# Kernel optimization log

Hardware: AMD Instinct MI355X
Metric: run time of the kernel (lower is better)

## Reference

```python
import jax, jax.numpy as jnp
import numpy as np

B, CIN, H, W = 16, 15, 256, 256
C, L, M = 64, 4, 16
ENV, D1D = 40, 4
HEAD_IN = C + ENV + D1D
BN_EPS = 1e-5


def setup_inputs() -> dict:
    key = jax.random.key(0)
    ks = iter(jax.random.split(key, 40))
    nrm = lambda shape: jax.random.normal(next(ks), shape, dtype=jnp.float32)
    scale = (2.0 / (C + C)) ** 0.5
    uni = lambda shape: scale * (jax.random.uniform(next(ks), shape, dtype=jnp.float32) - 0.5)
    d = {
        'grid': nrm((B, CIN, H, W)),
        'env': nrm((B, ENV)),
        'd1d': nrm((B, D1D)),
        'lift_w': nrm((C, CIN)) * 0.1, 'lift_b': nrm((C,)) * 0.01,
        'w1r': uni((L, C, C, M, M)), 'w1i': uni((L, C, C, M, M)),
        'w2r': uni((L, C, C, M, M)), 'w2i': uni((L, C, C, M, M)),
        'skip_w': nrm((L, C, C)) * 0.1, 'skip_b': nrm((L, C)) * 0.01,
        'bn_g': jnp.ones((L, C)), 'bn_b': jnp.zeros((L, C)),
        'bn_m': nrm((L, C)) * 0.01, 'bn_v': jnp.abs(nrm((L, C))) * 0.1 + 1.0,
        'proj_w': nrm((C, C)) * 0.1, 'proj_b': nrm((C,)) * 0.01,
        'dw1': nrm((128, HEAD_IN)) * 0.05, 'db1': nrm((128,)) * 0.01,
        'dw2': nrm((64, 128)) * 0.05, 'db2': nrm((64,)) * 0.01,
        'dw3': nrm((8, 64)) * 0.05, 'db3': nrm((8,)) * 0.01,
        'iw1': nrm((128, HEAD_IN)) * 0.05, 'ib1': nrm((128,)) * 0.01,
        'iw2': nrm((64, 128)) * 0.05, 'ib2': nrm((64,)) * 0.01,
        'iw3': nrm((4, 64)) * 0.05, 'ib3': nrm((4,)) * 0.01,
    }
    return d


def _spectral(x, w1, w2):
    # x: [B,C,H,W] real; w1,w2: [C,C,M,M] complex
    h, w = x.shape[-2], x.shape[-1]
    xft = jnp.fft.rfft2(x)  # [B,C,H,W//2+1] complex
    top = jnp.einsum('bixy,ioxy->boxy', xft[:, :, :M, :M], w1)
    bot = jnp.einsum('bixy,ioxy->boxy', xft[:, :, -M:, :M], w2)
    out_ft = jnp.zeros(xft.shape, dtype=xft.dtype)
    out_ft = out_ft.at[:, :, :M, :M].set(top).at[:, :, h - M:, :M].set(bot)
    return jnp.fft.irfft2(out_ft, s=(h, w))


def _conv1x1(x, w, b):
    return jnp.einsum('bchw,oc->bohw', x, w) + b[None, :, None, None]


def _gelu(x):
    return jax.nn.gelu(x, approximate=False)


def reference(grid, env, d1d, lift_w, lift_b, w1r, w1i, w2r, w2i, skip_w, skip_b,
              bn_g, bn_b, bn_m, bn_v, proj_w, proj_b,
              dw1, db1, dw2, db2, dw3, db3, iw1, ib1, iw2, ib2, iw3, ib3):
    x = _gelu(_conv1x1(grid, lift_w, lift_b))
    for l in range(L):
        residual = x
        w1 = w1r[l] + 1j * w1i[l]
        w2 = w2r[l] + 1j * w2i[l]
        y = _spectral(x, w1, w2) + _conv1x1(x, skip_w[l], skip_b[l])
        # BatchNorm2d in eval mode (running stats), dropout is identity at eval
        y = (y - bn_m[l][None, :, None, None]) * jax.lax.rsqrt(bn_v[l] + BN_EPS)[None, :, None, None]
        y = y * bn_g[l][None, :, None, None] + bn_b[l][None, :, None, None]
        x = _gelu(y) + residual
    x = _gelu(_conv1x1(x, proj_w, proj_b))
    x = x.mean(axis=(-2, -1))  # [B,C]
    x = jnp.concatenate([x, env, d1d], axis=-1)  # [B, C+44]
    h = _gelu(x @ dw1.T + db1)
    h = _gelu(h @ dw2.T + db2)
    out_dir = h @ dw3.T + db3
    g = _gelu(x @ iw1.T + ib1)
    g = _gelu(g @ iw2.T + ib2)
    out_int = g @ iw3.T + ib3
    return out_dir, out_int
```

## Files before the change

### kernel.cpp

```cpp
#include <hip/hip_runtime.h>
#include <hip/hip_bf16.h>
#include <math.h>

#define B_ 16
#define CIN_ 15
#define C_ 64
#define L_ 4

typedef __attribute__((ext_vector_type(8))) short short8;
typedef __attribute__((ext_vector_type(4))) short short4v;
typedef __attribute__((ext_vector_type(4))) float f32x4;

__device__ __forceinline__ float gelu_f(float x) {
    float z = fabsf(x) * 0.70710678118654752440f;
    float t = __builtin_amdgcn_rcpf(fmaf(0.3275911f, z, 1.0f));
    float p = t * fmaf(t, fmaf(t, fmaf(t, fmaf(t, 1.061405429f, -1.453152027f), 1.421413741f), -0.284496736f), 0.254829592f);
    float e = __expf(-z * z);
    float E = fmaf(-p, e, 1.0f);
    return 0.5f * fmaf(fabsf(x), E, x);
}

__device__ __forceinline__ unsigned short f2bf(float x) {
    __hip_bfloat16 h = __float2bfloat16(x);
    return *(unsigned short*)&h;
}
__device__ __forceinline__ float bf2f(unsigned short u) {
    __hip_bfloat16 h = *(__hip_bfloat16*)&u;
    return __bfloat162float(h);
}
__device__ __forceinline__ f32x4 mfma16(short8 a, short8 b, f32x4 c) {
    return __builtin_amdgcn_mfma_f32_16x16x32_bf16(a, b, c, 0, 0, 0);
}

#define TWO_PI_OVER_256 0.024543692606170259674f

__global__ __launch_bounds__(256) void k_prep(const float* __restrict__ skip_w,
                                              const float* __restrict__ bn_g, const float* __restrict__ bn_v,
                                              const float* __restrict__ proj_w, const float* __restrict__ lift_w,
                                              unsigned short* __restrict__ TfH, unsigned short* __restrict__ TfL,
                                              unsigned short* __restrict__ TiH, unsigned short* __restrict__ TiL,
                                              unsigned short* __restrict__ WH, unsigned short* __restrict__ WL,
                                              unsigned short* __restrict__ PH, unsigned short* __restrict__ PL,
                                              unsigned short* __restrict__ FcH, unsigned short* __restrict__ FcL,
                                              unsigned short* __restrict__ FsH, unsigned short* __restrict__ FsL,
                                              unsigned short* __restrict__ FnH, unsigned short* __restrict__ FnL,
                                              unsigned short* __restrict__ IcH, unsigned short* __restrict__ IcL,
                                              unsigned short* __restrict__ IsH, unsigned short* __restrict__ IsL,
                                              unsigned short* __restrict__ InH, unsigned short* __restrict__ InL,
                                              unsigned short* __restrict__ LwH, unsigned short* __restrict__ LwL) {
    int id = blockIdx.x * 256 + threadIdx.x;
    if (id < 8192) {
        int col = id >> 8, w = id & 255;
        int kk = (col < 16) ? col : (col - 16);
        float s, c;
        sincosf(TWO_PI_OVER_256 * (float)((w * kk) & 255), &s, &c);
        float v = (col < 16) ? c : -s;
        unsigned short hi = f2bf(v);
        TfH[id] = hi; TfL[id] = f2bf(v - bf2f(hi));
    } else if (id < 16384) {
        int idx = id - 8192;
        int w = idx >> 5, k = idx & 31, ky = k >> 1;
        float s, c;
        sincosf(TWO_PI_OVER_256 * (float)((w * ky) & 255), &s, &c);
        float v = (k & 1) ? -s : c;
        unsigned short hi = f2bf(v);
        TiH[idx] = hi; TiL[idx] = f2bf(v - bf2f(hi));
    } else if (id < 32768) {
        int idx = id - 16384;
        int lco = idx >> 6;
        float scl = bn_g[lco] * rsqrtf(bn_v[lco] + 1e-5f);
        float v = scl * skip_w[idx];
        unsigned short hi = f2bf(v);
        WH[idx] = hi; WL[idx] = f2bf(v - bf2f(hi));
    } else if (id < 36864) {
        int idx = id - 32768;
        float v = proj_w[idx];
        unsigned short hi = f2bf(v);
        PH[idx] = hi; PL[idx] = f2bf(v - bf2f(hi));
    } else if (id < 45056) {
        int idx = id - 36864;
        int j = idx >> 8, h = idx & 255;
        int kxu = j + ((j < 16) ? 0 : 224);
        float s, c;
        sincosf(TWO_PI_OVER_256 * (float)((h * kxu) & 255), &s, &c);
        unsigned short ch = f2bf(c);
        FcH[idx] = ch; FcL[idx] = f2bf(c - bf2f(ch));
        unsigned short sh = f2bf(s);
        unsigned short sl = f2bf(s - bf2f(sh));
        FsH[idx] = sh; FsL[idx] = sl;
        FnH[idx] = sh ^ 0x8000; FnL[idx] = sl ^ 0x8000;
    } else if (id < 53248) {
        int idx = id - 45056;
        int h = idx >> 5, j = idx & 31;
        int kxu = j + ((j < 16) ? 0 : 224);
        float s, c;
        sincosf(TWO_PI_OVER_256 * (float)((h * kxu) & 255), &s, &c);
        unsigned short ch = f2bf(c);
        IcH[idx] = ch; IcL[idx] = f2bf(c - bf2f(ch));
        unsigned short sh = f2bf(s);
        unsigned short sl = f2bf(s - bf2f(sh));
        IsH[idx] = sh; IsL[idx] = sl;
        InH[idx] = sh ^ 0x8000; InL[idx] = sl ^ 0x8000;
    } else if (id < 55296) {
        int idx = id - 53248;
        int co = idx >> 5, k = idx & 31;
        float v = (k < CIN_) ? lift_w[co * CIN_ + k] : 0.0f;
        unsigned short hi = f2bf(v);
        LwH[idx] = hi; LwL[idx] = f2bf(v - bf2f(hi));
    }
}

__global__ __launch_bounds__(256) void k_lift(const float* __restrict__ g,
                                              const unsigned short* __restrict__ LwH, const unsigned short* __restrict__ LwL,
                                              const float* __restrict__ lb, unsigned short* __restrict__ X,
                                              const unsigned short* __restrict__ TfH, const unsigned short* __restrict__ TfL,
                                              float2* __restrict__ Y) {
    __shared__ unsigned short xl[64 * 264];
    __shared__ float lbs[C_];
    int b = blockIdx.x >> 8, h = blockIdx.x & 255;
    int t = threadIdx.x;
    if (t < C_) lbs[t] = lb[t];
    int wv = t >> 6, ln = t & 63;
    int lx = ln & 15, q = ln >> 4;
    short8 bwh[4], bwl[4];
    #pragma unroll
    for (int mt = 0; mt < 4; mt++) {
        bwh[mt] = *(const short8*)(LwH + (mt * 16 + lx) * 32 + q * 8);
        bwl[mt] = *(const short8*)(LwL + (mt * 16 + lx) * 32 + q * 8);
    }
    __syncthreads();
    const float* gb = g + ((size_t)(b * CIN_) * 256 + h) * 256;
    #pragma unroll 1
    for (int nt = 0; nt < 4; nt++) {
        int w0 = wv * 64 + nt * 16;
        int w = w0 + lx;
        short8 agh = {0, 0, 0, 0, 0, 0, 0, 0};
        short8 agl = {0, 0, 0, 0, 0, 0, 0, 0};
        #pragma unroll
        for (int j = 0; j < 8; j++) {
            int ci = q * 8 + j;
            if (ci < CIN_) {
                float v = gb[(size_t)ci * 65536 + w];
                unsigned short hv = f2bf(v);
                agh[j] = (short)hv;
                agl[j] = (short)f2bf(v - bf2f(hv));
            }
        }
        f32x4 acc[4];
        #pragma unroll
        for (int mt = 0; mt < 4; mt++) acc[mt] = (f32x4){0.f, 0.f, 0.f, 0.f};
        #pragma unroll
        for (int mt = 0; mt < 4; mt++) {
            acc[mt] = mfma16(agh, bwh[mt], acc[mt]);
            acc[mt] = mfma16(agh, bwl[mt], acc[mt]);
            acc[mt] = mfma16(agl, bwh[mt], acc[mt]);
        }
        #pragma unroll
        for (int mt = 0; mt < 4; mt++) {
            int co = mt * 16 + lx;
            float bias = lbs[co];
            short4v nw;
            #pragma unroll
            for (int r = 0; r < 4; r++)
                nw[r] = (short)f2bf(gelu_f(acc[mt][r] + bias));
            *(short4v*)(&xl[co * 264 + w0 + q * 4]) = nw;
        }
    }
    __syncthreads();
    {
        f32x4 fa0 = {0.f, 0.f, 0.f, 0.f}, fa1 = {0.f, 0.f, 0.f, 0.f};
        for (int ks = 0; ks < 8; ks++) {
            int k0 = ks * 32;
            short8 a = *(const short8*)(&xl[(wv * 16 + lx) * 264 + k0 + q * 8]);
            short8 bh0 = *(const short8*)(TfH + lx * 256 + k0 + q * 8);
            short8 bl0 = *(const short8*)(TfL + lx * 256 + k0 + q * 8);
            short8 bh1 = *(const short8*)(TfH + (16 + lx) * 256 + k0 + q * 8);
            short8 bl1 = *(const short8*)(TfL + (16 + lx) * 256 + k0 + q * 8);
            fa0 = mfma16(a, bh0, fa0); fa0 = mfma16(a, bl0, fa0);
            fa1 = mfma16(a, bh1, fa1); fa1 = mfma16(a, bl1, fa1);
        }
        #pragma unroll
        for (int r = 0; r < 4; r++) {
            int c = wv * 16 + q * 4 + r;
            Y[(b * 64 + c) * 4096 + h * 16 + lx] = make_float2(fa0[r], fa1[r]);
        }
    }
    unsigned short* Xg = X + (size_t)(b * 256 + h) * 16384;
    #pragma unroll
    for (int r = 0; r < 8; r++) {
        int idx = r * 256 + t;
        int c = idx >> 5, w8 = idx & 31;
        *(short8*)(Xg + idx * 8) = *(const short8*)(&xl[c * 264 + w8 * 8]);
    }
}

__global__ __launch_bounds__(256) void k_fwd_h(const float2* __restrict__ Y, float2* __restrict__ XF,
                                               const unsigned short* __restrict__ FcH, const unsigned short* __restrict__ FcL,
                                               const unsigned short* __restrict__ FsH, const unsigned short* __restrict__ FsL,
                                               const unsigned short* __restrict__ FnH, const unsigned short* __restrict__ FnL) {
    __shared__ float red[4][2][2][64][4];
    int bc = blockIdx.x;
    int t = threadIdx.x;
    int wv = t >> 6, l = t & 63, lx = l & 15, g = l >> 4;
    const float2* Yb = Y + (size_t)bc * 4096;
    f32x4 aR[2], aI[2];
    aR[0] = (f32x4){0.f,0.f,0.f,0.f}; aR[1] = aR[0]; aI[0] = aR[0]; aI[1] = aR[0];
    #pragma unroll
    for (int kk = 0; kk < 2; kk++) {
        int ks = wv * 2 + kk;
        short8 yrh, yrl, yih, yil;
        #pragma unroll
        for (int j = 0; j < 8; j++) {
            float2 v = Yb[(ks * 32 + g * 8 + j) * 16 + lx];
            unsigned short h1 = f2bf(v.x);
            yrh[j] = (short)h1; yrl[j] = (short)f2bf(v.x - bf2f(h1));
            unsigned short h2 = f2bf(v.y);
            yih[j] = (short)h2; yil[j] = (short)f2bf(v.y - bf2f(h2));
        }
        #pragma unroll
        for (int rt = 0; rt < 2; rt++) {
            int base = (rt * 16 + lx) * 256 + ks * 32 + g * 8;
            short8 ch = *(const short8*)(FcH + base);
            short8 cl = *(const short8*)(FcL + base);
            short8 sh = *(const short8*)(FsH + base);
            short8 sl = *(const short8*)(FsL + base);
            short8 nh = *(const short8*)(FnH + base);
            short8 nl = *(const short8*)(FnL + base);
            aR[rt] = mfma16(ch, yrh, aR[rt]);
            aR[rt] = mfma16(ch, yrl, aR[rt]);
            aR[rt] = mfma16(cl, yrh, aR[rt]);
            aR[rt] = mfma16(sh, yih, aR[rt]);
            aR[rt] = mfma16(sh, yil, aR[rt]);
            aR[rt] = mfma16(sl, yih, aR[rt]);
            aI[rt] = mfma16(ch, yih, aI[rt]);
            aI[rt] = mfma16(ch, yil, aI[rt]);
            aI[rt] = mfma16(cl, yih, aI[rt]);
            aI[rt] = mfma16(nh, yrh, aI[rt]);
            aI[rt] = mfma16(nh, yrl, aI[rt]);
            aI[rt] = mfma16(nl, yrh, aI[rt]);
        }
    }
    #pragma unroll
    for (int rt = 0; rt < 2; rt++) {
        *(f32x4*)&red[wv][rt][0][l][0] = aR[rt];
        *(f32x4*)&red[wv][rt][1][l][0] = aI[rt];
    }
    __syncthreads();
    if (t < 128) {
        int rt = t >> 6, ll = t & 63;
        int llx = ll & 15, gg = ll >> 4;
        f32x4 R = *(const f32x4*)&red[0][rt][0][ll][0];
        f32x4 I = *(const f32x4*)&red[0][rt][1][ll][0];
        #pragma unroll
        for (int w = 1; w < 4; w++) {
            R += *(const f32x4*)&red[w][rt][0][ll][0];
            I += *(const f32x4*)&red[w][rt][1][ll][0];
        }
        #pragma unroll
        for (int r = 0; r < 4; r++) {
            int j = rt * 16 + gg * 4 + r;
            XF[(j * 16 + llx) * 1024 + bc] = make_float2(R[r], I[r]);
        }
    }
}

__global__ __launch_bounds__(256) void k_repack(const float* __restrict__ w1r, const float* __restrict__ w1i,
                                                const float* __restrict__ w2r, const float* __restrict__ w2i,
                                                float2* __restrict__ WPK, int l) {
    int j = blockIdx.x >> 6, i = blockIdx.x & 63;
    int t = threadIdx.x;
    int ky = t & 15, o0 = (t >> 4) * 4;
    int x = j & 15;
    const float* wr = (j < 16) ? w1r : w2r;
    const float* wi = (j < 16) ? w1i : w2i;
    size_t sb = ((size_t)(l * 64 + i) * 64 + o0) * 256 + x * 16 + ky;
    float r0 = wr[sb];       float v0 = wi[sb];
    float r1 = wr[sb + 256]; float v1 = wi[sb + 256];
    float r2 = wr[sb + 512]; float v2 = wi[sb + 512];
    float r3 = wr[sb + 768]; float v3 = wi[sb + 768];
    float4* dst = (float4*)(WPK + ((size_t)(j * 16 + ky) * 64 + i) * 64 + o0);
    dst[0] = make_float4(r0, v0, r1, v1);
    dst[1] = make_float4(r2, v2, r3, v3);
}

__global__ __launch_bounds__(256) void k_mix(const float2* __restrict__ XF, const float2* __restrict__ WPK,
                                             float2* __restrict__ YF) {
    __shared__ float2 xs[1024];
    __shared__ float2 wls[4096];
    int s = blockIdx.x;
    int t = threadIdx.x;
    for (int idx = t; idx < 1024; idx += 256) xs[idx] = XF[s * 1024 + idx];
    for (int idx = t; idx < 4096; idx += 256) wls[idx] = WPK[(size_t)s * 4096 + idx];
    __syncthreads();
    int o = t & 63, bg = t >> 6;
    float2 acc[4];
    #pragma unroll
    for (int q = 0; q < 4; q++) acc[q] = make_float2(0.f, 0.f);
    for (int i = 0; i < 64; i++) {
        float2 wv = wls[i * 64 + o];
        #pragma unroll
        for (int q = 0; q < 4; q++) {
            float2 xv = xs[(bg * 4 + q) * 64 + i];
            acc[q].x += xv.x * wv.x - xv.y * wv.y;
            acc[q].y += xv.x * wv.y + xv.y * wv.x;
        }
    }
    #pragma unroll
    for (int q = 0; q < 4; q++) {
        int b = bg * 4 + q;
        YF[(b * 64 + o) * 512 + s] = acc[q];
    }
}

__global__ __launch_bounds__(256) void k_inv_h(const float2* __restrict__ YF, float2* __restrict__ Z,
                                               const unsigned short* __restrict__ IcH, const unsigned short* __restrict__ IcL,
                                               const unsigned short* __restrict__ IsH, const unsigned short* __restrict__ IsL,
                                               const unsigned short* __restrict__ InH, const unsigned short* __restrict__ InL) {
    int bc = blockIdx.x;
    int t = threadIdx.x;
    int wv = t >> 6, l = t & 63, lx = l & 15, g = l >> 4;
    const float2* Yb = YF + (size_t)bc * 512;
    short8 xrh, xrl, xih, xil;
    #pragma unroll
    for (int jj = 0; jj < 8; jj++) {
        float2 v = Yb[(g * 8 + jj) * 16 + lx];
        unsigned short h1 = f2bf(v.x);
        xrh[jj] = (short)h1; xrl[jj] = (short)f2bf(v.x - bf2f(h1));
        unsigned short h2 = f2bf(v.y);
        xih[jj] = (short)h2; xil[jj] = (short)f2bf(v.y - bf2f(h2));
    }
    float2* Zb = Z + (size_t)bc * 4096;
    #pragma unroll
    for (int hh = 0; hh < 4; hh++) {
        int ht = wv * 4 + hh;
        int base = (ht * 16 + lx) * 32 + g * 8;
        short8 ch = *(const short8*)(IcH + base);
        short8 cl = *(const short8*)(IcL + base);
        short8 sh = *(const short8*)(IsH + base);
        short8 sl = *(const short8*)(IsL + base);
        short8 nh = *(const short8*)(InH + base);
        short8 nl = *(const short8*)(InL + base);
        f32x4 aR = {0.f,0.f,0.f,0.f}, aI = {0.f,0.f,0.f,0.f};
        aR = mfma16(ch, xrh, aR); aR = mfma16(ch, xrl, aR); aR = mfma16(cl, xrh, aR);
        aR = mfma16(nh, xih, aR); aR = mfma16(nh, xil, aR); aR = mfma16(nl, xih, aR);
        aI = mfma16(sh, xrh, aI); aI = mfma16(sh, xrl, aI); aI = mfma16(sl, xrh, aI);
        aI = mfma16(ch, xih, aI); aI = mfma16(ch, xil, aI); aI = mfma16(cl, xih, aI);
        #pragma unroll
        for (int r = 0; r < 4; r++) {
            int h = ht * 16 + g * 4 + r;
            Zb[h * 16 + lx] = make_float2(aR[r], aI[r]);
        }
    }
}

__global__ __launch_bounds__(256) void k_tail(unsigned short* __restrict__ X, const float2* __restrict__ Z,
                                              const unsigned short* __restrict__ WH, const unsigned short* __restrict__ WL,
                                              const float* __restrict__ sbl, const float* __restrict__ bng,
                                              const float* __restrict__ bnb, const float* __restrict__ bnm,
                                              const float* __restrict__ bnv,
                                              const unsigned short* __restrict__ TiH, const unsigned short* __restrict__ TiL,
                                              const unsigned short* __restrict__ TfH, const unsigned short* __restrict__ TfL,
                                              float2* __restrict__ Y, int mode,
                                              const unsigned short* __restrict__ PH, const unsigned short* __restrict__ PL,
                                              const float* __restrict__ pb, float* __restrict__ ACC) {
    __shared__ unsigned short xl[64 * 264];
    __shared__ float cbs[64];
    __shared__ float pacc[64];
    __shared__ float pbs[64];
    int b = blockIdx.x >> 8, h = blockIdx.x & 255;
    int t = threadIdx.x;
    unsigned short* Xg = X + (size_t)(b * 256 + h) * 16384;
    #pragma unroll
    for (int r = 0; r < 8; r++) {
        int idx = r * 256 + t;
        int c = idx >> 5, w8 = idx & 31;
        *(short8*)(&xl[c * 264 + w8 * 8]) = *(const short8*)(Xg + idx * 8);
    }
    if (t < 64) {
        float scl = bng[t] * rsqrtf(bnv[t] + 1e-5f);
        cbs[t] = scl * (sbl[t] - bnm[t]) + bnb[t];
        pacc[t] = 0.f;
        pbs[t] = pb[t];
    }
    __syncthreads();

    int wv = t >> 6, ln = t & 63;
    int lx = ln & 15, q = ln >> 4;

    short8 azh[4], azl[4];
    {
        const float2* Zg = Z + (size_t)(b * 64) * 4096 + h * 16;
        #pragma unroll
        for (int mt = 0; mt < 4; mt++) {
            int co = mt * 16 + lx;
            float scl = bng[co] * rsqrtf(bnv[co] + 1e-5f);
            float f2v = scl * (2.0f / 65536.0f);
            float f0 = (q == 0) ? (scl * (1.0f / 65536.0f)) : f2v;
            const float4* zp = (const float4*)(Zg + (size_t)co * 4096 + q * 4);
            float4 z0 = zp[0], z1 = zp[1];
            float v[8];
            v[0] = z0.x * f0;  v[1] = z0.y * f0;
            v[2] = z0.z * f2v; v[3] = z0.w * f2v;
            v[4] = z1.x * f2v; v[5] = z1.y * f2v;
            v[6] = z1.z * f2v; v[7] = z1.w * f2v;
            #pragma unroll
            for (int j = 0; j < 8; j++) {
                unsigned short hv = f2bf(v[j]);
                azh[mt][j] = (short)hv;
                azl[mt][j] = (short)f2bf(v[j] - bf2f(hv));
            }
        }
    }

    short8 tah = *(const short8*)(TiH + (wv * 64 + lx) * 32 + q * 8);
    short8 tal = *(const short8*)(TiL + (wv * 64 + lx) * 32 + q * 8);
    #pragma unroll 1
    for (int nt = 0; nt < 4; nt++) {
        int w0 = wv * 64 + nt * 16;
        int w = w0 + lx;
        short8 tah_c = tah, tal_c = tal;
        if (nt < 3) {
            tah = *(const short8*)(TiH + (w + 16) * 32 + q * 8);
            tal = *(const short8*)(TiL + (w + 16) * 32 + q * 8);
        }
        f32x4 acc[4];
        #pragma unroll
        for (int mt = 0; mt < 4; mt++) acc[mt] = (f32x4){0.f, 0.f, 0.f, 0.f};
        #pragma unroll
        for (int mt = 0; mt < 4; mt++) {
            acc[mt] = mfma16(tah_c, azh[mt], acc[mt]);
            acc[mt] = mfma16(tah_c, azl[mt], acc[mt]);
            acc[mt] = mfma16(tal_c, azh[mt], acc[mt]);
        }
        #pragma unroll
        for (int ks = 0; ks < 2; ks++) {
            int k0 = ks * 32;
            short8 afr;
            #pragma unroll
            for (int j = 0; j < 8; j++)
                afr[j] = (short)xl[(k0 + q * 8 + j) * 264 + w];
            #pragma unroll
            for (int mt = 0; mt < 4; mt++) {
                short8 bh = *(const short8*)(WH + (mt * 16 + lx) * 64 + k0 + q * 8);
                short8 bl = *(const short8*)(WL + (mt * 16 + lx) * 64 + k0 + q * 8);
                acc[mt] = mfma16(afr, bh, acc[mt]);
                acc[mt] = mfma16(afr, bl, acc[mt]);
            }
        }
        #pragma unroll
        for (int mt = 0; mt < 4; mt++) {
            int co = mt * 16 + lx;
            float cb = cbs[co];
            unsigned short* xp = &xl[co * 264 + w0 + q * 4];
            short4v old = *(const short4v*)xp;
            short4v nw;
            #pragma unroll
            for (int r = 0; r < 4; r++) {
                float y = acc[mt][r] + cb;
                float v = gelu_f(y) + bf2f((unsigned short)old[r]);
                nw[r] = (short)f2bf(v);
            }
            *(short4v*)xp = nw;
        }
    }
    __syncthreads();

    if (mode == 1) {
        f32x4 fa0 = {0.f, 0.f, 0.f, 0.f}, fa1 = {0.f, 0.f, 0.f, 0.f};
        for (int ks = 0; ks < 8; ks++) {
            int k0 = ks * 32;
            short8 a = *(const short8*)(&xl[(wv * 16 + lx) * 264 + k0 + q * 8]);
            short8 bh0 = *(const short8*)(TfH + lx * 256 + k0 + q * 8);
            short8 bl0 = *(const short8*)(TfL + lx * 256 + k0 + q * 8);
            short8 bh1 = *(const short8*)(TfH + (16 + lx) * 256 + k0 + q * 8);
            short8 bl1 = *(const short8*)(TfL + (16 + lx) * 256 + k0 + q * 8);
            fa0 = mfma16(a, bh0, fa0); fa0 = mfma16(a, bl0, fa0);
            fa1 = mfma16(a, bh1, fa1); fa1 = mfma16(a, bl1, fa1);
        }
        #pragma unroll
        for (int r = 0; r < 4; r++) {
            int c = wv * 16 + q * 4 + r;
            Y[(b * 64 + c) * 4096 + h * 16 + lx] = make_float2(fa0[r], fa1[r]);
        }
        #pragma unroll
        for (int r = 0; r < 8; r++) {
            int idx = r * 256 + t;
            int c = idx >> 5, w8 = idx & 31;
            *(short8*)(Xg + idx * 8) = *(const short8*)(&xl[c * 264 + w8 * 8]);
        }
    } else {
        float psum[4][4];
        #pragma unroll
        for (int mt = 0; mt < 4; mt++)
            #pragma unroll
            for (int r = 0; r < 4; r++) psum[mt][r] = 0.f;
        #pragma unroll 1
        for (int nt = 0; nt < 4; nt++) {
            int w = wv * 64 + nt * 16 + lx;
            f32x4 acc[4];
            #pragma unroll
            for (int mt = 0; mt < 4; mt++) acc[mt] = (f32x4){0.f, 0.f, 0.f, 0.f};
            #pragma unroll
            for (int ks = 0; ks < 2; ks++) {
                int k0 = ks * 32;
                short8 afr;
                #pragma unroll
                for (int j = 0; j < 8; j++)
                    afr[j] = (short)xl[(k0 + q * 8 + j) * 264 + w];
                #pragma unroll
                for (int mt = 0; mt < 4; mt++) {
                    short8 bh = *(const short8*)(PH + (mt * 16 + lx) * 64 + k0 + q * 8);
                    short8 bl = *(const short8*)(PL + (mt * 16 + lx) * 64 + k0 + q * 8);
                    acc[mt] = mfma16(afr, bh, acc[mt]);
                    acc[mt] = mfma16(afr, bl, acc[mt]);
                }
            }
            #pragma unroll
            for (int mt = 0; mt < 4; mt++) {
                int co = mt * 16 + lx;
                #pragma unroll
                for (int r = 0; r < 4; r++)
                    psum[mt][r] += gelu_f(acc[mt][r] + pbs[co]);
            }
        }
        #pragma unroll
        for (int mt = 0; mt < 4; mt++) {
            int co = mt * 16 + lx;
            float s = psum[mt][0] + psum[mt][1] + psum[mt][2] + psum[mt][3];
            s += __shfl_xor(s, 16, 64);
            s += __shfl_xor(s, 32, 64);
            if (q == 0) atomicAdd(&pacc[co], s);
        }
        __syncthreads();
        if (t < 64) atomicAdd(&ACC[b * 64 + t], pacc[t]);
    }
}

__global__ __launch_bounds__(128) void k_head(const float* __restrict__ ACC, const float* __restrict__ env,
                                              const float* __restrict__ d1d,
                                              const float* __restrict__ dw1, const float* __restrict__ db1,
                                              const float* __restrict__ dw2, const float* __restrict__ db2,
                                              const float* __restrict__ dw3, const float* __restrict__ db3,
                                              const float* __restrict__ iw1, const float* __restrict__ ib1,
                                              const float* __restrict__ iw2, const float* __restrict__ ib2,
                                              const float* __restrict__ iw3, const float* __restrict__ ib3,
                                              float* __restrict__ out) {
    __shared__ float xc[108];
    __shared__ float h1[128];
    __shared__ float h2[64];
    int b = blockIdx.x, t = threadIdx.x;
    if (t < 64) xc[t] = ACC[b * 64 + t] * (1.0f / 65536.0f);
    else if (t < 104) xc[t] = env[b * 40 + (t - 64)];
    else if (t < 108) xc[t] = d1d[b * 4 + (t - 104)];
    __syncthreads();
    {
        float a = db1[t];
        for (int k = 0; k < 108; k++) a += xc[k] * dw1[t * 108 + k];
        h1[t] = gelu_f(a);
    }
    __syncthreads();
    if (t < 64) {
        float a = db2[t];
        for (int k = 0; k < 128; k++) a += h1[k] * dw2[t * 128 + k];
        h2[t] = gelu_f(a);
    }
    __syncthreads();
    if (t < 8) {
        float a = db3[t];
        for (int k = 0; k < 64; k++) a += h2[k] * dw3[t * 64 + k];
        out[b * 8 + t] = a;
    }
    __syncthreads();
    {
        float a = ib1[t];
        for (int k = 0; k < 108; k++) a += xc[k] * iw1[t * 108 + k];
        h1[t] = gelu_f(a);
    }
    __syncthreads();
    if (t < 64) {
        float a = ib2[t];
        for (int k = 0; k < 128; k++) a += h1[k] * iw2[t * 128 + k];
        h2[t] = gelu_f(a);
    }
    __syncthreads();
    if (t < 4) {
        float a = ib3[t];
        for (int k = 0; k < 64; k++) a += h2[k] * iw3[t * 64 + k];
        out[128 + b * 4 + t] = a;
    }
}

extern "C" void kernel_launch(void* const* d_in, const int* in_sizes, int n_in,
                              void* d_out, int out_size, void* d_ws, size_t ws_size,
                              hipStream_t stream) {
    const float* grid_  = (const float*)d_in[0];
    const float* env    = (const float*)d_in[1];
    const float* d1d    = (const float*)d_in[2];
    const float* lift_w = (const float*)d_in[3];
    const float* lift_b = (const float*)d_in[4];
    const float* w1r    = (const float*)d_in[5];
    const float* w1i    = (const float*)d_in[6];
    const float* w2r    = (const float*)d_in[7];
    const float* w2i    = (const float*)d_in[8];
    const float* skip_w = (const float*)d_in[9];
    const float* skip_b = (const float*)d_in[10];
    const float* bn_g   = (const float*)d_in[11];
    const float* bn_b   = (const float*)d_in[12];
    const float* bn_m   = (const float*)d_in[13];
    const float* bn_v   = (const float*)d_in[14];
    const float* proj_w = (const float*)d_in[15];
    const float* proj_b = (const float*)d_in[16];
    const float* dw1 = (const float*)d_in[17];
    const float* db1 = (const float*)d_in[18];
    const float* dw2 = (const float*)d_in[19];
    const float* db2 = (const float*)d_in[20];
    const float* dw3 = (const float*)d_in[21];
    const float* db3 = (const float*)d_in[22];
    const float* iw1 = (const float*)d_in[23];
    const float* ib1 = (const float*)d_in[24];
    const float* iw2 = (const float*)d_in[25];
    const float* ib2 = (const float*)d_in[26];
    const float* iw3 = (const float*)d_in[27];
    const float* ib3 = (const float*)d_in[28];

    char* ws = (char*)d_ws;
    unsigned short* X   = (unsigned short*)(ws);
    float2* S   = (float2*)(ws + 134217728);
    float2* XF  = (float2*)(ws + 167772160);
    float2* YF  = (float2*)(ws + 171966464);
    float2* WPK = (float2*)(ws + 176160768);
    float*  ACC = (float*)(ws + 192937984);
    unsigned short* TfH = (unsigned short*)(ws + 192942080);
    unsigned short* TfL = (unsigned short*)(ws + 192958464);
    unsigned short* TiH = (unsigned short*)(ws + 192974848);
    unsigned short* TiL = (unsigned short*)(ws + 192991232);
    unsigned short* WH  = (unsigned short*)(ws + 193007616);
    unsigned short* WL  = (unsigned short*)(ws + 193040384);
    unsigned short* PH  = (unsigned short*)(ws + 193073152);
    unsigned short* PL  = (unsigned short*)(ws + 193081344);
    unsigned short* FcH = (unsigned short*)(ws + 193089536);
    unsigned short* FcL = (unsigned short*)(ws + 193105920);
    unsigned short* FsH = (unsigned short*)(ws + 193122304);
    unsigned short* FsL = (unsigned short*)(ws + 193138688);
    unsigned short* FnH = (unsigned short*)(ws + 193155072);
    unsigned short* FnL = (unsigned short*)(ws + 193171456);
    unsigned short* IcH = (unsigned short*)(ws + 193187840);
    unsigned short* IcL = (unsigned short*)(ws + 193204224);
    unsigned short* IsH = (unsigned short*)(ws + 193220608);
    unsigned short* IsL = (unsigned short*)(ws + 193236992);
    unsigned short* InH = (unsigned short*)(ws + 193253376);
    unsigned short* InL = (unsigned short*)(ws + 193269760);
    unsigned short* LwH = (unsigned short*)(ws + 193286144);
    unsigned short* LwL = (unsigned short*)(ws + 193290240);

    hipMemsetAsync(ACC, 0, 1024 * sizeof(float), stream);
    k_prep<<<216, 256, 0, stream>>>(skip_w, bn_g, bn_v, proj_w, lift_w,
                                    TfH, TfL, TiH, TiL, WH, WL, PH, PL,
                                    FcH, FcL, FsH, FsL, FnH, FnL, IcH, IcL, IsH, IsL, InH, InL,
                                    LwH, LwL);
    k_lift<<<4096, 256, 0, stream>>>(grid_, LwH, LwL, lift_b, X, TfH, TfL, S);
    for (int l = 0; l < L_; l++) {
        k_repack<<<2048, 256, 0, stream>>>(w1r, w1i, w2r, w2i, WPK, l);
        k_fwd_h<<<1024, 256, 0, stream>>>(S, XF, FcH, FcL, FsH, FsL, FnH, FnL);
        k_mix<<<512, 256, 0, stream>>>(XF, WPK, YF);
        k_inv_h<<<1024, 256, 0, stream>>>(YF, S, IcH, IcL, IsH, IsL, InH, InL);
        k_tail<<<4096, 256, 0, stream>>>(X, S, WH + l * 4096, WL + l * 4096,
                                         skip_b + l * 64, bn_g + l * 64, bn_b + l * 64,
                                         bn_m + l * 64, bn_v + l * 64,
                                         TiH, TiL, TfH, TfL, S, (l < 3) ? 1 : 2,
                                         PH, PL, proj_b, ACC);
    }
    k_head<<<16, 128, 0, stream>>>(ACC, env, d1d, dw1, db1, dw2, db2, dw3, db3,
                                   iw1, ib1, iw2, ib2, iw3, ib3, (float*)d_out);
}
```

Measured before the change: 1.121 ms.

## Split lift across channel halves and pre-split BN-scaled bf16 in inverse FFT

```diff
diff --git a/kernel.cpp b/kernel.cpp
--- a/kernel.cpp
+++ b/kernel.cpp
@@ -115,18 +115,19 @@
                                               const float* __restrict__ lb, unsigned short* __restrict__ X,
                                               const unsigned short* __restrict__ TfH, const unsigned short* __restrict__ TfL,
                                               float2* __restrict__ Y) {
-    __shared__ unsigned short xl[64 * 264];
+    __shared__ unsigned short xl[32 * 264];
     __shared__ float lbs[C_];
-    int b = blockIdx.x >> 8, h = blockIdx.x & 255;
+    int b = blockIdx.x >> 9, h = (blockIdx.x >> 1) & 255, ch = blockIdx.x & 1;
     int t = threadIdx.x;
     if (t < C_) lbs[t] = lb[t];
     int wv = t >> 6, ln = t & 63;
     int lx = ln & 15, q = ln >> 4;
-    short8 bwh[4], bwl[4];
-    #pragma unroll
-    for (int mt = 0; mt < 4; mt++) {
-        bwh[mt] = *(const short8*)(LwH + (mt * 16 + lx) * 32 + q * 8);
-        bwl[mt] = *(const short8*)(LwL + (mt * 16 + lx) * 32 + q * 8);
+    int cob = ch * 32;
+    short8 bwh[2], bwl[2];
+    #pragma unroll
+    for (int mt = 0; mt < 2; mt++) {
+        bwh[mt] = *(const short8*)(LwH + (cob + mt * 16 + lx) * 32 + q * 8);
+        bwl[mt] = *(const short8*)(LwL + (cob + mt * 16 + lx) * 32 + q * 8);
     }
     __syncthreads();
     const float* gb = g + ((size_t)(b * CIN_) * 256 + h) * 256;
@@ -146,28 +147,28 @@
                 agl[j] = (short)f2bf(v - bf2f(hv));
             }
         }
-        f32x4 acc[4];
-        #pragma unroll
-        for (int mt = 0; mt < 4; mt++) acc[mt] = (f32x4){0.f, 0.f, 0.f, 0.f};
-        #pragma unroll
-        for (int mt = 0; mt < 4; mt++) {
+        f32x4 acc[2];
+        #pragma unroll
+        for (int mt = 0; mt < 2; mt++) acc[mt] = (f32x4){0.f, 0.f, 0.f, 0.f};
+        #pragma unroll
+        for (int mt = 0; mt < 2; mt++) {
             acc[mt] = mfma16(agh, bwh[mt], acc[mt]);
             acc[mt] = mfma16(agh, bwl[mt], acc[mt]);
             acc[mt] = mfma16(agl, bwh[mt], acc[mt]);
         }
         #pragma unroll
-        for (int mt = 0; mt < 4; mt++) {
-            int co = mt * 16 + lx;
-            float bias = lbs[co];
+        for (int mt = 0; mt < 2; mt++) {
+            int cl = mt * 16 + lx;
+            float bias = lbs[cob + cl];
             short4v nw;
             #pragma unroll
             for (int r = 0; r < 4; r++)
                 nw[r] = (short)f2bf(gelu_f(acc[mt][r] + bias));
-            *(short4v*)(&xl[co * 264 + w0 + q * 4]) = nw;
-        }
-    }
-    __syncthreads();
-    {
+            *(short4v*)(&xl[cl * 264 + w0 + q * 4]) = nw;
+        }
+    }
+    __syncthreads();
+    if (wv < 2) {
         f32x4 fa0 = {0.f, 0.f, 0.f, 0.f}, fa1 = {0.f, 0.f, 0.f, 0.f};
         for (int ks = 0; ks < 8; ks++) {
             int k0 = ks * 32;
@@ -181,13 +182,13 @@
         }
         #pragma unroll
         for (int r = 0; r < 4; r++) {
-            int c = wv * 16 + q * 4 + r;
+            int c = cob + wv * 16 + q * 4 + r;
             Y[(b * 64 + c) * 4096 + h * 16 + lx] = make_float2(fa0[r], fa1[r]);
         }
     }
-    unsigned short* Xg = X + (size_t)(b * 256 + h) * 16384;
-    #pragma unroll
-    for (int r = 0; r < 8; r++) {
+    unsigned short* Xg = X + (size_t)(b * 256 + h) * 16384 + ch * 8192;
+    #pragma unroll
+    for (int r = 0; r < 4; r++) {
         int idx = r * 256 + t;
         int c = idx >> 5, w8 = idx & 31;
         *(short8*)(Xg + idx * 8) = *(const short8*)(&xl[c * 264 + w8 * 8]);
@@ -312,10 +313,11 @@
     }
 }
 
-__global__ __launch_bounds__(256) void k_inv_h(const float2* __restrict__ YF, float2* __restrict__ Z,
+__global__ __launch_bounds__(256) void k_inv_h(const float2* __restrict__ YF, unsigned short* __restrict__ Zs,
                                                const unsigned short* __restrict__ IcH, const unsigned short* __restrict__ IcL,
                                                const unsigned short* __restrict__ IsH, const unsigned short* __restrict__ IsL,
-                                               const unsigned short* __restrict__ InH, const unsigned short* __restrict__ InL) {
+                                               const unsigned short* __restrict__ InH, const unsigned short* __restrict__ InL,
+                                               const float* __restrict__ bng, const float* __restrict__ bnv) {
     int bc = blockIdx.x;
     int t = threadIdx.x;
     int wv = t >> 6, l = t & 63, lx = l & 15, g = l >> 4;
@@ -329,7 +331,9 @@
         unsigned short h2 = f2bf(v.y);
         xih[jj] = (short)h2; xil[jj] = (short)f2bf(v.y - bf2f(h2));
     }
-    float2* Zb = Z + (size_t)bc * 4096;
+    int c = bc & 63;
+    float s = bng[c] * rsqrtf(bnv[c] + 1e-5f) * ((lx == 0) ? (1.0f / 65536.0f) : (2.0f / 65536.0f));
+    unsigned short* Zb = Zs + (size_t)bc * 16384;
     #pragma unroll
     for (int hh = 0; hh < 4; hh++) {
         int ht = wv * 4 + hh;
@@ -348,12 +352,16 @@
         #pragma unroll
         for (int r = 0; r < 4; r++) {
             int h = ht * 16 + g * 4 + r;
-            Zb[h * 16 + lx] = make_float2(aR[r], aI[r]);
-        }
-    }
-}
-
-__global__ __launch_bounds__(256) void k_tail(unsigned short* __restrict__ X, const float2* __restrict__ Z,
+            float vR = aR[r] * s, vI = aI[r] * s;
+            unsigned short hR = f2bf(vR), hI = f2bf(vI);
+            unsigned short lR = f2bf(vR - bf2f(hR)), lI = f2bf(vI - bf2f(hI));
+            ((unsigned int*)(Zb + h * 64))[lx]      = (unsigned)hR | ((unsigned)hI << 16);
+            ((unsigned int*)(Zb + h * 64 + 32))[lx] = (unsigned)lR | ((unsigned)lI << 16);
+        }
+    }
+}
+
+__global__ __launch_bounds__(256) void k_tail(unsigned short* __restrict__ X, const unsigned short* __restrict__ Zs,
                                               const unsigned short* __restrict__ WH, const unsigned short* __restrict__ WL,
                                               const float* __restrict__ sbl, const float* __restrict__ bng,
                                               const float* __restrict__ bnb, const float* __restrict__ bnm,
@@ -389,26 +397,12 @@
 
     short8 azh[4], azl[4];
     {
-        const float2* Zg = Z + (size_t)(b * 64) * 4096 + h * 16;
+        const unsigned short* Zg = Zs + (size_t)(b * 64) * 16384 + h * 64;
         #pragma unroll
         for (int mt = 0; mt < 4; mt++) {
-            int co = mt * 16 + lx;
-            float scl = bng[co] * rsqrtf(bnv[co] + 1e-5f);
-            float f2v = scl * (2.0f / 65536.0f);
-            float f0 = (q == 0) ? (scl * (1.0f / 65536.0f)) : f2v;
-            const float4* zp = (const float4*)(Zg + (size_t)co * 4096 + q * 4);
-            float4 z0 = zp[0], z1 = zp[1];
-            float v[8];
-            v[0] = z0.x * f0;  v[1] = z0.y * f0;
-            v[2] = z0.z * f2v; v[3] = z0.w * f2v;
-            v[4] = z1.x * f2v; v[5] = z1.y * f2v;
-            v[6] = z1.z * f2v; v[7] = z1.w * f2v;
-            #pragma unroll
-            for (int j = 0; j < 8; j++) {
-                unsigned short hv = f2bf(v[j]);
-                azh[mt][j] = (short)hv;
-                azl[mt][j] = (short)f2bf(v[j] - bf2f(hv));
-            }
+            const unsigned short* zp = Zg + (size_t)(mt * 16 + lx) * 16384 + q * 8;
+            azh[mt] = *(const short8*)(zp);
+            azl[mt] = *(const short8*)(zp + 32);
         }
     }
 
@@ -653,18 +647,21 @@
     unsigned short* LwH = (unsigned short*)(ws + 193286144);
     unsigned short* LwL = (unsigned short*)(ws + 193290240);
 
+    unsigned short* Zs = (unsigned short*)S;
+
     hipMemsetAsync(ACC, 0, 1024 * sizeof(float), stream);
     k_prep<<<216, 256, 0, stream>>>(skip_w, bn_g, bn_v, proj_w, lift_w,
                                     TfH, TfL, TiH, TiL, WH, WL, PH, PL,
                                     FcH, FcL, FsH, FsL, FnH, FnL, IcH, IcL, IsH, IsL, InH, InL,
                                     LwH, LwL);
-    k_lift<<<4096, 256, 0, stream>>>(grid_, LwH, LwL, lift_b, X, TfH, TfL, S);
+    k_lift<<<8192, 256, 0, stream>>>(grid_, LwH, LwL, lift_b, X, TfH, TfL, S);
     for (int l = 0; l < L_; l++) {
         k_repack<<<2048, 256, 0, stream>>>(w1r, w1i, w2r, w2i, WPK, l);
         k_fwd_h<<<1024, 256, 0, stream>>>(S, XF, FcH, FcL, FsH, FsL, FnH, FnL);
         k_mix<<<512, 256, 0, stream>>>(XF, WPK, YF);
-        k_inv_h<<<1024, 256, 0, stream>>>(YF, S, IcH, IcL, IsH, IsL, InH, InL);
-        k_tail<<<4096, 256, 0, stream>>>(X, S, WH + l * 4096, WL + l * 4096,
+        k_inv_h<<<1024, 256, 0, stream>>>(YF, Zs, IcH, IcL, IsH, IsL, InH, InL,
+                                          bn_g + l * 64, bn_v + l * 64);
+        k_tail<<<4096, 256, 0, stream>>>(X, Zs, WH + l * 4096, WL + l * 4096,
                                          skip_b + l * 64, bn_g + l * 64, bn_b + l * 64,
                                          bn_m + l * 64, bn_v + l * 64,
                                          TiH, TiL, TfH, TfL, S, (l < 3) ? 1 : 2,
```

Result: no change. 1.121 ms (+0.1%).
